# Kernel optimization log

Hardware: AMD Instinct MI355X
Metric: run time of the kernel (lower is better)

## Reference

```python
import jax, jax.numpy as jnp
import numpy as np

ROWS, COLS = 1024, 1024
N_NODES = ROWS * COLS
RHO_W = 1000.0      # water density
RHO_I = 917.0       # ice density (unused in output path, kept for fidelity)
GRAV = 9.81
SEC_PER_A = 31556926.0
FLOW_COEFF = 0.0405
FLOW_EXP = 1.25     # 5/4
N_ITERS = 32        # fixed-point iterations for MFD flow accumulation


def _raster_links(rows, cols):
    ids = np.arange(rows * cols, dtype=np.int32).reshape(rows, cols)
    src_h = ids[:, :-1].ravel(); dst_h = ids[:, 1:].ravel()
    src_v = ids[:-1, :].ravel(); dst_v = ids[1:, :].ravel()
    return (np.concatenate([src_h, src_v]), np.concatenate([dst_h, dst_v]))


def setup_inputs() -> dict:
    key = jax.random.key(0)
    k1, k2, k3, k4 = jax.random.split(key, 4)
    melt_rate = jax.random.uniform(k1, (N_NODES,), jnp.float32) * 10.0          # m/a
    bedrock_elevation = jax.random.normal(k2, (N_NODES,), jnp.float32) * 500.0  # m
    water_pressure = jax.random.uniform(k3, (N_NODES,), jnp.float32) * 1.0e6    # Pa
    cell_area = jnp.full((N_NODES,), 1.0e4, jnp.float32)                        # 100m cells
    conduit_size = jax.random.uniform(k4, (N_NODES,), jnp.float32) + 0.01
    # landlab-style status: 0 = core node, 1 = fixed-value boundary (perimeter)
    status = np.zeros((ROWS, COLS), dtype=np.int32)
    status[0, :] = 1; status[-1, :] = 1; status[:, 0] = 1; status[:, -1] = 1
    src, dst = _raster_links(ROWS, COLS)
    return {
        "melt_rate": melt_rate,
        "bedrock_elevation": bedrock_elevation,
        "water_pressure": water_pressure,
        "cell_area": cell_area,
        "conduit_size": conduit_size,
        "status_at_node": jnp.asarray(status.ravel()),
        "link_src": jnp.asarray(src),
        "link_dst": jnp.asarray(dst),
    }


def reference(melt_rate, bedrock_elevation, water_pressure, cell_area,
              conduit_size, status_at_node, link_src, link_dst):
    n = melt_rate.shape[0]
    seg = lambda d, i: jax.ops.segment_sum(d, i, num_segments=n)

    # hydraulic potential (surface FlowDirectorMFD routes on)
    phi = RHO_W * GRAV * bedrock_elevation + water_pressure
    # local runoff input at each node
    runoff = melt_rate * cell_area / SEC_PER_A

    # MFD: split each node's outflow among downslope neighbors, proportional
    # to the positive potential drop along each link (unit link length).
    core = (status_at_node == 0)
    dphi = phi[link_src] - phi[link_dst]
    drop_fwd = jnp.maximum(dphi, 0.0) * core[link_src]   # src -> dst
    drop_bwd = jnp.maximum(-dphi, 0.0) * core[link_dst]  # dst -> src
    total_drop = seg(drop_fwd, link_src) + seg(drop_bwd, link_dst)
    s_safe = jnp.where(total_drop > 0.0, total_drop, 1.0)
    frac_fwd = drop_fwd / s_safe[link_src]
    frac_bwd = drop_bwd / s_safe[link_dst]

    # flow accumulation on the drainage DAG: Q = runoff + P^T Q (fixed-point)
    def step(q, _):
        inflow = seg(frac_fwd * q[link_src], link_dst) + seg(frac_bwd * q[link_dst], link_src)
        return runoff + inflow, None

    discharge, _ = jax.lax.scan(step, runoff, None, length=N_ITERS)

    # calc_hydraulic_gradient, masked to core nodes (status == 0)
    gradient = (discharge * FLOW_COEFF * conduit_size ** FLOW_EXP) ** 2
    return jnp.where(status_at_node == 0, gradient, 0.0)
```

## Files before the change

### kernel.cpp

```cpp
#include <hip/hip_runtime.h>

#define ROWS 1024
#define COLS 1024
#define NN (ROWS*COLS)

#define OT    16
#define HALO  8
#define TPD   (COLS/OT)
#define WPB   4
#define NT    (WPB*64)
#define NBLK  ((TPD*TPD)/WPB)

static constexpr float RHOG    = 1000.0f * 9.81f;
static constexpr float INV_SEC = 1.0f / 31556926.0f;
static constexpr float FLOWC   = 0.0405f;

__device__ __forceinline__ float4 gld4(const float* __restrict__ p, int g, bool in) {
    if (in) return *reinterpret_cast<const float4*>(p + g);
    return make_float4(0.f, 0.f, 0.f, 0.f);
}

__global__ __launch_bounds__(256) void k_pre(
        const float* __restrict__ bed, const float* __restrict__ pw,
        const int* __restrict__ status,
        const float* __restrict__ melt, const float* __restrict__ area,
        float* __restrict__ phi, float* __restrict__ inv,
        float* __restrict__ runoff) {
    int i = blockIdx.x * 256 + threadIdx.x;
    int r = i >> 10, c = i & (COLS - 1);
    float p = RHOG * bed[i] + pw[i];
    float t = 0.f;
    if (c > 0)        t += fmaxf(p - (RHOG * bed[i - 1]    + pw[i - 1]),    0.f);
    if (c < COLS - 1) t += fmaxf(p - (RHOG * bed[i + 1]    + pw[i + 1]),    0.f);
    if (r > 0)        t += fmaxf(p - (RHOG * bed[i - COLS] + pw[i - COLS]), 0.f);
    if (r < ROWS - 1) t += fmaxf(p - (RHOG * bed[i + COLS] + pw[i + COLS]), 0.f);
    phi[i]    = p;
    inv[i]    = (status[i] == 0 && t > 0.f) ? (1.f / t) : 0.f;
    runoff[i] = melt[i] * area[i] * INV_SEC;
}

template <bool FIRST, bool FINAL>
__global__ __launch_bounds__(NT, 3) void k_step(
        const float* __restrict__ phi_g, const float* __restrict__ inv_g,
        const float* __restrict__ run_g, const float* __restrict__ qin,
        float* __restrict__ qout,
        const float* __restrict__ cond, const int* __restrict__ status) {
    const int tid  = threadIdx.x;
    const int lane = tid & 63;
    const int wid  = blockIdx.x * WPB + (tid >> 6);
    const int tr = wid >> 6, tc = wid & (TPD - 1);
    const int R0 = tr * OT - HALO, C0 = tc * OT - HALO;
    const int wr = lane >> 3, wc = lane & 7;
    const int gr0 = R0 + wr * 4, gc0 = C0 + wc * 4;

    const int upL = (wr > 0) ? lane - 8 : lane;
    const int dnL = (wr < 7) ? lane + 8 : lane;
    const int lfL = (wc > 0) ? lane - 1 : lane;
    const int rtL = (wc < 7) ? lane + 1 : lane;

    const bool cin = ((unsigned)gc0 < COLS);

    float ph[4][4], iv[4][4];
#pragma unroll
    for (int i = 0; i < 4; ++i) {
        bool in = ((unsigned)(gr0 + i) < ROWS) & cin;
        int  g  = (gr0 + i) * COLS + gc0;
        float4 p4 = gld4(phi_g, g, in);
        float4 i4 = gld4(inv_g, g, in);
        ph[i][0]=p4.x; ph[i][1]=p4.y; ph[i][2]=p4.z; ph[i][3]=p4.w;
        iv[i][0]=i4.x; iv[i][1]=i4.y; iv[i][2]=i4.z; iv[i][3]=i4.w;
    }

    float phU[4], phD[4], ivU[4], ivD[4], phL[4], phR[4], ivL[4], ivR[4];
#pragma unroll
    for (int j = 0; j < 4; ++j) {
        phU[j] = __shfl(ph[3][j], upL, 64);  ivU[j] = __shfl(iv[3][j], upL, 64);
        phD[j] = __shfl(ph[0][j], dnL, 64);  ivD[j] = __shfl(iv[0][j], dnL, 64);
    }
#pragma unroll
    for (int i = 0; i < 4; ++i) {
        phL[i] = __shfl(ph[i][3], lfL, 64);  ivL[i] = __shfl(iv[i][3], lfL, 64);
        phR[i] = __shfl(ph[i][0], rtL, 64);  ivR[i] = __shfl(iv[i][0], rtL, 64);
    }

    float WH[4][4];
    float WV[4][4];
    float EH[4];
    float SV[4];
#pragma unroll
    for (int i = 0; i < 4; ++i)
#pragma unroll
        for (int j = 0; j < 4; ++j) {
            float pw_ = (j > 0) ? ph[i][j-1] : phL[i];
            float iw_ = (j > 0) ? iv[i][j-1] : ivL[i];
            float s   = pw_ - ph[i][j];
            WH[i][j]  = s * ((s > 0.f) ? iw_ : iv[i][j]);
            float pn_ = (i > 0) ? ph[i-1][j] : phU[j];
            float in_ = (i > 0) ? iv[i-1][j] : ivU[j];
            float sv  = pn_ - ph[i][j];
            WV[i][j]  = sv * ((sv > 0.f) ? in_ : iv[i][j]);
        }
#pragma unroll
    for (int i = 0; i < 4; ++i) {
        float s = ph[i][3] - phR[i];
        EH[i] = s * ((s > 0.f) ? iv[i][3] : ivR[i]);
    }
#pragma unroll
    for (int j = 0; j < 4; ++j) {
        float s = ph[3][j] - phD[j];
        SV[j] = s * ((s > 0.f) ? iv[3][j] : ivD[j]);
    }

    float q[4][4], ro[4][4];
#pragma unroll
    for (int i = 0; i < 4; ++i) {
        bool in = ((unsigned)(gr0 + i) < ROWS) & cin;
        int  g  = (gr0 + i) * COLS + gc0;
        float4 r4 = gld4(run_g, g, in);
        ro[i][0]=r4.x; ro[i][1]=r4.y; ro[i][2]=r4.z; ro[i][3]=r4.w;
        if (FIRST) {
            q[i][0]=r4.x; q[i][1]=r4.y; q[i][2]=r4.z; q[i][3]=r4.w;
        } else {
            float4 q4 = gld4(qin, g, in);
            q[i][0]=q4.x; q[i][1]=q4.y; q[i][2]=q4.z; q[i][3]=q4.w;
        }
    }

#pragma unroll 1
    for (int s = 0; s < HALO; ++s) {
        float u[4], d[4], l[4], r[4];
#pragma unroll
        for (int j = 0; j < 4; ++j) {
            u[j] = __shfl(q[3][j], upL, 64);
            d[j] = __shfl(q[0][j], dnL, 64);
        }
#pragma unroll
        for (int i = 0; i < 4; ++i) {
            l[i] = __shfl(q[i][3], lfL, 64);
            r[i] = __shfl(q[i][0], rtL, 64);
        }
        float nq[4][4];
#pragma unroll
        for (int i = 0; i < 4; ++i)
#pragma unroll
            for (int j = 0; j < 4; ++j) {
                float qw = (j > 0) ? q[i][j-1] : l[i];
                float qe = (j < 3) ? q[i][j+1] : r[i];
                float qn = (i > 0) ? q[i-1][j] : u[j];
                float qs = (i < 3) ? q[i+1][j] : d[j];
                float We = (j < 3) ? WH[i][j+1] : EH[i];
                float Ws = (i < 3) ? WV[i+1][j] : SV[j];
                float a = ro[i][j];
                a = fmaf(fmaxf(WH[i][j], 0.f), qw, a);
                a = fmaf(fmaxf(-We,      0.f), qe, a);
                a = fmaf(fmaxf(WV[i][j], 0.f), qn, a);
                a = fmaf(fmaxf(-Ws,      0.f), qs, a);
                nq[i][j] = a;
            }
#pragma unroll
        for (int i = 0; i < 4; ++i)
#pragma unroll
            for (int j = 0; j < 4; ++j) q[i][j] = nq[i][j];
    }

    if ((wr >= 2) & (wr < 6) & (wc >= 2) & (wc < 6)) {
#pragma unroll
        for (int i = 0; i < 4; ++i) {
            int go = (gr0 + i) * COLS + gc0;
            if (FINAL) {
                float4 c4 = *reinterpret_cast<const float4*>(cond + go);
                int4 st   = *reinterpret_cast<const int4*>(status + go);
                float4 o;
                float t;
                t = q[i][0] * FLOWC * (c4.x * sqrtf(sqrtf(c4.x))); o.x = (st.x == 0) ? t * t : 0.f;
                t = q[i][1] * FLOWC * (c4.y * sqrtf(sqrtf(c4.y))); o.y = (st.y == 0) ? t * t : 0.f;
                t = q[i][2] * FLOWC * (c4.z * sqrtf(sqrtf(c4.z))); o.z = (st.z == 0) ? t * t : 0.f;
                t = q[i][3] * FLOWC * (c4.w * sqrtf(sqrtf(c4.w))); o.w = (st.w == 0) ? t * t : 0.f;
                *reinterpret_cast<float4*>(qout + go) = o;
            } else {
                *reinterpret_cast<float4*>(qout + go) =
                    make_float4(q[i][0], q[i][1], q[i][2], q[i][3]);
            }
        }
    }
}

extern "C" void kernel_launch(void* const* d_in, const int* in_sizes, int n_in,
                              void* d_out, int out_size, void* d_ws, size_t ws_size,
                              hipStream_t stream) {
    const float* melt   = (const float*)d_in[0];
    const float* bed    = (const float*)d_in[1];
    const float* pw     = (const float*)d_in[2];
    const float* area   = (const float*)d_in[3];
    const float* cond   = (const float*)d_in[4];
    const int*   status = (const int*)d_in[5];
    float* out = (float*)d_out;

    char* ws = (char*)d_ws;
    float* phi    = (float*)(ws);
    float* inv    = (float*)(ws + 4ull  * NN);
    float* runoff = (float*)(ws + 8ull  * NN);
    float* qA     = (float*)(ws + 12ull * NN);
    float* qB     = (float*)(ws + 16ull * NN);

    k_pre<<<dim3(NN / 256), dim3(256), 0, stream>>>(bed, pw, status, melt, area,
                                                    phi, inv, runoff);

    dim3 grid(NBLK), block(NT);
    k_step<true,  false><<<grid, block, 0, stream>>>(phi, inv, runoff, runoff, qA, nullptr, nullptr);
    k_step<false, false><<<grid, block, 0, stream>>>(phi, inv, runoff, qA, qB, nullptr, nullptr);
    k_step<false, false><<<grid, block, 0, stream>>>(phi, inv, runoff, qB, qA, nullptr, nullptr);
    k_step<false, true ><<<grid, block, 0, stream>>>(phi, inv, runoff, qA, out, cond, status);
}
```

Measured before the change: 150.1 us.

## Fuse the four halo-step kernels into one cooperative kernel with grid syncs

Replaces the four separate k_step launches with a single cooperative kernel. Each wave keeps its phi, inv and link-weight registers across all stages, and the stages are separated by grid-wide syncs with ping-pong global buffers. This is meant to remove repeated kernel launches and the repeated reload and recomputation of the potential-derived weights. It requires all 1024 blocks to be resident at once (four per CU under launch_bounds(NT,4)), which may force register spills. If the cooperative launch fails, it falls back to the old four-launch path.

```diff
diff --git a/kernel.cpp b/kernel.cpp
--- a/kernel.cpp
+++ b/kernel.cpp
@@ -1,4 +1,7 @@
 #include <hip/hip_runtime.h>
+#include <hip/hip_cooperative_groups.h>
+
+namespace cg = cooperative_groups;
 
 #define ROWS 1024
 #define COLS 1024
@@ -39,6 +42,168 @@
     runoff[i] = melt[i] * area[i] * INV_SEC;
 }
 
+
+__global__ __launch_bounds__(NT, 4) void k_coop(
+        const float* __restrict__ phi_g, const float* __restrict__ inv_g,
+        const float* __restrict__ run_g,
+        float* __restrict__ qA, float* __restrict__ qB,
+        float* __restrict__ out,
+        const float* __restrict__ cond, const int* __restrict__ status) {
+    const int tid  = threadIdx.x;
+    const int lane = tid & 63;
+    const int wid  = blockIdx.x * WPB + (tid >> 6);
+    const int tr = wid >> 6, tc = wid & (TPD - 1);
+    const int R0 = tr * OT - HALO, C0 = tc * OT - HALO;
+    const int wr = lane >> 3, wc = lane & 7;
+    const int gr0 = R0 + wr * 4, gc0 = C0 + wc * 4;
+
+    const int upL = (wr > 0) ? lane - 8 : lane;
+    const int dnL = (wr < 7) ? lane + 8 : lane;
+    const int lfL = (wc > 0) ? lane - 1 : lane;
+    const int rtL = (wc < 7) ? lane + 1 : lane;
+
+    const bool cin = ((unsigned)gc0 < COLS);
+    const bool central = (wr >= 2) & (wr < 6) & (wc >= 2) & (wc < 6);
+
+    float ph[4][4], iv[4][4];
+#pragma unroll
+    for (int i = 0; i < 4; ++i) {
+        bool in = ((unsigned)(gr0 + i) < ROWS) & cin;
+        int  g  = (gr0 + i) * COLS + gc0;
+        float4 p4 = gld4(phi_g, g, in);
+        float4 i4 = gld4(inv_g, g, in);
+        ph[i][0]=p4.x; ph[i][1]=p4.y; ph[i][2]=p4.z; ph[i][3]=p4.w;
+        iv[i][0]=i4.x; iv[i][1]=i4.y; iv[i][2]=i4.z; iv[i][3]=i4.w;
+    }
+
+    float phU[4], phD[4], ivU[4], ivD[4], phL[4], phR[4], ivL[4], ivR[4];
+#pragma unroll
+    for (int j = 0; j < 4; ++j) {
+        phU[j] = __shfl(ph[3][j], upL, 64);  ivU[j] = __shfl(iv[3][j], upL, 64);
+        phD[j] = __shfl(ph[0][j], dnL, 64);  ivD[j] = __shfl(iv[0][j], dnL, 64);
+    }
+#pragma unroll
+    for (int i = 0; i < 4; ++i) {
+        phL[i] = __shfl(ph[i][3], lfL, 64);  ivL[i] = __shfl(iv[i][3], lfL, 64);
+        phR[i] = __shfl(ph[i][0], rtL, 64);  ivR[i] = __shfl(iv[i][0], rtL, 64);
+    }
+
+    float WH[4][4];
+    float WV[4][4];
+    float EH[4];
+    float SV[4];
+#pragma unroll
+    for (int i = 0; i < 4; ++i)
+#pragma unroll
+        for (int j = 0; j < 4; ++j) {
+            float pw_ = (j > 0) ? ph[i][j-1] : phL[i];
+            float iw_ = (j > 0) ? iv[i][j-1] : ivL[i];
+            float s   = pw_ - ph[i][j];
+            WH[i][j]  = s * ((s > 0.f) ? iw_ : iv[i][j]);
+            float pn_ = (i > 0) ? ph[i-1][j] : phU[j];
+            float in_ = (i > 0) ? iv[i-1][j] : ivU[j];
+            float sv  = pn_ - ph[i][j];
+            WV[i][j]  = sv * ((sv > 0.f) ? in_ : iv[i][j]);
+        }
+#pragma unroll
+    for (int i = 0; i < 4; ++i) {
+        float s = ph[i][3] - phR[i];
+        EH[i] = s * ((s > 0.f) ? iv[i][3] : ivR[i]);
+    }
+#pragma unroll
+    for (int j = 0; j < 4; ++j) {
+        float s = ph[3][j] - phD[j];
+        SV[j] = s * ((s > 0.f) ? iv[3][j] : ivD[j]);
+    }
+
+    float q[4][4], ro[4][4];
+#pragma unroll
+    for (int i = 0; i < 4; ++i) {
+        bool in = ((unsigned)(gr0 + i) < ROWS) & cin;
+        int  g  = (gr0 + i) * COLS + gc0;
+        float4 r4 = gld4(run_g, g, in);
+        ro[i][0]=r4.x; ro[i][1]=r4.y; ro[i][2]=r4.z; ro[i][3]=r4.w;
+        q[i][0]=r4.x;  q[i][1]=r4.y;  q[i][2]=r4.z;  q[i][3]=r4.w;
+    }
+
+    cg::grid_group gg = cg::this_grid();
+
+#pragma unroll 1
+    for (int stage = 0; stage < 4; ++stage) {
+#pragma unroll 1
+        for (int s = 0; s < HALO; ++s) {
+            float u[4], d[4], l[4], r[4];
+#pragma unroll
+            for (int j = 0; j < 4; ++j) {
+                u[j] = __shfl(q[3][j], upL, 64);
+                d[j] = __shfl(q[0][j], dnL, 64);
+            }
+#pragma unroll
+            for (int i = 0; i < 4; ++i) {
+                l[i] = __shfl(q[i][3], lfL, 64);
+                r[i] = __shfl(q[i][0], rtL, 64);
+            }
+            float nq[4][4];
+#pragma unroll
+            for (int i = 0; i < 4; ++i)
+#pragma unroll
+                for (int j = 0; j < 4; ++j) {
+                    float qw = (j > 0) ? q[i][j-1] : l[i];
+                    float qe = (j < 3) ? q[i][j+1] : r[i];
+                    float qn = (i > 0) ? q[i-1][j] : u[j];
+                    float qs = (i < 3) ? q[i+1][j] : d[j];
+                    float We = (j < 3) ? WH[i][j+1] : EH[i];
+                    float Ws = (i < 3) ? WV[i+1][j] : SV[j];
+                    float a = ro[i][j];
+                    a = fmaf(fmaxf(WH[i][j], 0.f), qw, a);
+                    a = fmaf(fmaxf(-We,      0.f), qe, a);
+                    a = fmaf(fmaxf(WV[i][j], 0.f), qn, a);
+                    a = fmaf(fmaxf(-Ws,      0.f), qs, a);
+                    nq[i][j] = a;
+                }
+#pragma unroll
+            for (int i = 0; i < 4; ++i)
+#pragma unroll
+                for (int j = 0; j < 4; ++j) q[i][j] = nq[i][j];
+        }
+
+        if (stage < 3) {
+            float* dst = (stage & 1) ? qB : qA;
+            if (central) {
+#pragma unroll
+                for (int i = 0; i < 4; ++i) {
+                    int go = (gr0 + i) * COLS + gc0;
+                    *reinterpret_cast<float4*>(dst + go) =
+                        make_float4(q[i][0], q[i][1], q[i][2], q[i][3]);
+                }
+            }
+            gg.sync();
+            const float* src = (stage & 1) ? qB : qA;
+#pragma unroll
+            for (int i = 0; i < 4; ++i) {
+                bool in = ((unsigned)(gr0 + i) < ROWS) & cin;
+                int  g  = (gr0 + i) * COLS + gc0;
+                float4 q4 = gld4(src, g, in);
+                q[i][0]=q4.x; q[i][1]=q4.y; q[i][2]=q4.z; q[i][3]=q4.w;
+            }
+        } else if (central) {
+#pragma unroll
+            for (int i = 0; i < 4; ++i) {
+                int go = (gr0 + i) * COLS + gc0;
+                float4 c4 = *reinterpret_cast<const float4*>(cond + go);
+                int4 st   = *reinterpret_cast<const int4*>(status + go);
+                float4 o;
+                float t;
+                t = q[i][0] * FLOWC * (c4.x * sqrtf(sqrtf(c4.x))); o.x = (st.x == 0) ? t * t : 0.f;
+                t = q[i][1] * FLOWC * (c4.y * sqrtf(sqrtf(c4.y))); o.y = (st.y == 0) ? t * t : 0.f;
+                t = q[i][2] * FLOWC * (c4.z * sqrtf(sqrtf(c4.z))); o.z = (st.z == 0) ? t * t : 0.f;
+                t = q[i][3] * FLOWC * (c4.w * sqrtf(sqrtf(c4.w))); o.w = (st.w == 0) ? t * t : 0.f;
+                *reinterpret_cast<float4*>(out + go) = o;
+            }
+        }
+    }
+}
+
 template <bool FIRST, bool FINAL>
 __global__ __launch_bounds__(NT, 3) void k_step(
         const float* __restrict__ phi_g, const float* __restrict__ inv_g,
@@ -70,7 +235,6 @@
         ph[i][0]=p4.x; ph[i][1]=p4.y; ph[i][2]=p4.z; ph[i][3]=p4.w;
         iv[i][0]=i4.x; iv[i][1]=i4.y; iv[i][2]=i4.z; iv[i][3]=i4.w;
     }
-
     float phU[4], phD[4], ivU[4], ivD[4], phL[4], phR[4], ivL[4], ivR[4];
 #pragma unroll
     for (int j = 0; j < 4; ++j) {
@@ -82,11 +246,7 @@
         phL[i] = __shfl(ph[i][3], lfL, 64);  ivL[i] = __shfl(iv[i][3], lfL, 64);
         phR[i] = __shfl(ph[i][0], rtL, 64);  ivR[i] = __shfl(iv[i][0], rtL, 64);
     }
-
-    float WH[4][4];
-    float WV[4][4];
-    float EH[4];
-    float SV[4];
+    float WH[4][4], WV[4][4], EH[4], SV[4];
 #pragma unroll
     for (int i = 0; i < 4; ++i)
 #pragma unroll
@@ -110,7 +270,6 @@
         float s = ph[3][j] - phD[j];
         SV[j] = s * ((s > 0.f) ? iv[3][j] : ivD[j]);
     }
-
     float q[4][4], ro[4][4];
 #pragma unroll
     for (int i = 0; i < 4; ++i) {
@@ -125,7 +284,6 @@
             q[i][0]=q4.x; q[i][1]=q4.y; q[i][2]=q4.z; q[i][3]=q4.w;
         }
     }
-
 #pragma unroll 1
     for (int s = 0; s < HALO; ++s) {
         float u[4], d[4], l[4], r[4];
@@ -162,7 +320,6 @@
 #pragma unroll
             for (int j = 0; j < 4; ++j) q[i][j] = nq[i][j];
     }
-
     if ((wr >= 2) & (wr < 6) & (wc >= 2) & (wc < 6)) {
 #pragma unroll
         for (int i = 0; i < 4; ++i) {
@@ -206,9 +363,19 @@
     k_pre<<<dim3(NN / 256), dim3(256), 0, stream>>>(bed, pw, status, melt, area,
                                                     phi, inv, runoff);
 
-    dim3 grid(NBLK), block(NT);
-    k_step<true,  false><<<grid, block, 0, stream>>>(phi, inv, runoff, runoff, qA, nullptr, nullptr);
-    k_step<false, false><<<grid, block, 0, stream>>>(phi, inv, runoff, qA, qB, nullptr, nullptr);
-    k_step<false, false><<<grid, block, 0, stream>>>(phi, inv, runoff, qB, qA, nullptr, nullptr);
-    k_step<false, true ><<<grid, block, 0, stream>>>(phi, inv, runoff, qA, out, cond, status);
-}
+    void* kargs[] = {
+        (void*)&phi, (void*)&inv, (void*)&runoff,
+        (void*)&qA,  (void*)&qB,  (void*)&out,
+        (void*)&cond, (void*)&status
+    };
+    hipError_t e = hipLaunchCooperativeKernel((const void*)k_coop,
+                                              dim3(NBLK), dim3(NT),
+                                              kargs, 0, stream);
+    if (e != hipSuccess) {
+        dim3 grid(NBLK), block(NT);
+        k_step<true,  false><<<grid, block, 0, stream>>>(phi, inv, runoff, runoff, qA, nullptr, nullptr);
+        k_step<false, false><<<grid, block, 0, stream>>>(phi, inv, runoff, qA, qB, nullptr, nullptr);
+        k_step<false, false><<<grid, block, 0, stream>>>(phi, inv, runoff, qB, qA, nullptr, nullptr);
+        k_step<false, true ><<<grid, block, 0, stream>>>(phi, inv, runoff, qA, out, cond, status);
+    }
+}
```

New measurement: 571.4 us. 3.81x slower.
